# Optimization experiments

Hardware: AMD Instinct MI355X
Metric: run time of the kernel (lower is better)

Reference implementation:

```python
import jax, jax.numpy as jnp
import numpy as np

DIM = 128
CODEBOOK_SCALE = 16384
N_TOKENS = 16384


def setup_inputs() -> dict:
    key = jax.random.key(0)
    k1, k2 = jax.random.split(key)
    x = jax.random.normal(k1, (N_TOKENS, DIM), dtype=jnp.float32)
    codebook = jax.random.normal(k2, (CODEBOOK_SCALE, DIM), dtype=jnp.float32)
    return {"x": x, "codebook": codebook}


def reference(x, codebook):
    # scores: [N, codebook_scale] = x @ codebook.T
    scores = jnp.einsum("nd,cd->nc", x, codebook)
    indices = jnp.argmax(scores, axis=-1)  # [N] int
    loss = jnp.zeros((), dtype=jnp.float32)  # original returns constant 0.0 loss
    return (indices, loss)
```

## Files before the change

### kernel.cpp

```cpp
#include <hip/hip_runtime.h>
#include <hip/hip_bf16.h>

#define NT 16384
#define ND 128
#define NC 16384
#define NSPLIT 8
#define MARGIN 0.4f
#define TILE_BYTES 16384
#define NTILES 32

typedef __bf16 bf16x8 __attribute__((ext_vector_type(8)));
typedef unsigned short u16x8 __attribute__((ext_vector_type(8)));
typedef float f32x4 __attribute__((ext_vector_type(4)));

#define MF __builtin_amdgcn_mfma_f32_16x16x32_bf16

static __device__ __forceinline__ unsigned short f2bf(float f) {
    unsigned u = __float_as_uint(f);
    return (unsigned short)((u + 0x7FFFu + ((u >> 16) & 1u)) >> 16);
}
static __device__ __forceinline__ float bf2f(unsigned short u) {
    return __uint_as_float(((unsigned)u) << 16);
}
static __device__ __forceinline__ bf16x8 u2b(u16x8 u) {
    return __builtin_bit_cast(bf16x8, u);
}
static __device__ __forceinline__ void gl2lds(const void* g, void* l) {
    __builtin_amdgcn_global_load_lds(
        (const __attribute__((address_space(1))) unsigned int*)g,
        (__attribute__((address_space(3))) unsigned int*)l, 16, 0, 0);
}

__global__ __launch_bounds__(256) void lfq_convert_cb(
    const float4* __restrict__ cb4, unsigned short* __restrict__ cbs)
{
    const unsigned i = blockIdx.x * 256 + threadIdx.x;
    const unsigned c = i >> 4;
    const unsigned k = i & 15u;
    const float4 v0 = cb4[i * 2];
    const float4 v1 = cb4[i * 2 + 1];
    const unsigned tile = c >> 6, r = c & 63u;
    const unsigned pos  = (k + r) & 15u;
    u16x8 h;
    h[0] = f2bf(v0.x); h[1] = f2bf(v0.y); h[2] = f2bf(v0.z); h[3] = f2bf(v0.w);
    h[4] = f2bf(v1.x); h[5] = f2bf(v1.y); h[6] = f2bf(v1.z); h[7] = f2bf(v1.w);
    *(u16x8*)(cbs + tile * 8192u + r * 128u + pos * 8u) = h;
}

static __device__ __forceinline__ float exact_dot(
    const float4* __restrict__ xr4, const float* __restrict__ cf, int cidx)
{
    const float4* cr = (const float4*)(cf + (size_t)cidx * ND);
    float a0 = 0.f, a1 = 0.f, a2 = 0.f, a3 = 0.f;
#pragma unroll
    for (int i = 0; i < 32; i += 4) {
        float4 x0 = xr4[i+0], x1 = xr4[i+1], x2 = xr4[i+2], x3 = xr4[i+3];
        float4 c0 = cr[i+0],  c1 = cr[i+1],  c2 = cr[i+2],  c3 = cr[i+3];
        a0 += x0.x*c0.x + x0.y*c0.y + x0.z*c0.z + x0.w*c0.w;
        a1 += x1.x*c1.x + x1.y*c1.y + x1.z*c1.z + x1.w*c1.w;
        a2 += x2.x*c2.x + x2.y*c2.y + x2.z*c2.z + x2.w*c2.w;
        a3 += x3.x*c3.x + x3.y*c3.y + x3.z*c3.z + x3.w*c3.w;
    }
    return (a0 + a1) + (a2 + a3);
}

static __device__ __forceinline__ float exact_dot_g(
    const float* __restrict__ xf, const float* __restrict__ cf,
    int token, int cidx)
{
    const float4* xr = (const float4*)(xf + (size_t)token * ND);
    const float4* cr = (const float4*)(cf + (size_t)cidx * ND);
    float a0 = 0.f, a1 = 0.f, a2 = 0.f, a3 = 0.f;
#pragma unroll
    for (int i = 0; i < 32; i += 4) {
        float4 x0 = xr[i+0], x1 = xr[i+1], x2 = xr[i+2], x3 = xr[i+3];
        float4 c0 = cr[i+0], c1 = cr[i+1], c2 = cr[i+2], c3 = cr[i+3];
        a0 += x0.x*c0.x + x0.y*c0.y + x0.z*c0.z + x0.w*c0.w;
        a1 += x1.x*c1.x + x1.y*c1.y + x1.z*c1.z + x1.w*c1.w;
        a2 += x2.x*c2.x + x2.y*c2.y + x2.z*c2.z + x2.w*c2.w;
        a3 += x3.x*c3.x + x3.y*c3.y + x3.z*c3.z + x3.w*c3.w;
    }
    return (a0 + a1) + (a2 + a3);
}

static __device__ __forceinline__ void top2_upd(
    const f32x4& a, float* b1r, float* b2r, unsigned pk)
{
#pragma unroll
    for (int r4 = 0; r4 < 4; ++r4) {
        float p = __uint_as_float((__float_as_uint(a[r4]) & 0xFFFFFF80u) | pk);
        b2r[r4] = __builtin_amdgcn_fmed3f(p, b1r[r4], b2r[r4]);
        b1r[r4] = fmaxf(p, b1r[r4]);
    }
}

__global__ __launch_bounds__(256)
__attribute__((amdgpu_waves_per_eu(2, 2)))
void lfq_stage1(
    const float* __restrict__ xf, const unsigned short* __restrict__ cbs,
    float* __restrict__ sb1, float* __restrict__ sb2,
    int* __restrict__ si1, int* __restrict__ si2)
{
    const int split = blockIdx.x & 7;
    const int tb    = blockIdx.x >> 3;
    const int t0    = tb * 256;
    const int tid   = threadIdx.x;
    const int w     = tid >> 6;
    const int lane  = tid & 63;
    const int n     = lane & 15;
    const int quad  = lane >> 4;

    __shared__ __attribute__((aligned(16))) unsigned char lds[2 * TILE_BYTES];

    bf16x8 ah[4][4];
#pragma unroll
    for (int tt = 0; tt < 4; ++tt) {
        const float* xr = xf + (size_t)(t0 + w * 64 + tt * 16 + n) * ND + quad * 8;
#pragma unroll
        for (int kk = 0; kk < 4; ++kk) {
            float4 v0 = *(const float4*)(xr + kk * 32);
            float4 v1 = *(const float4*)(xr + kk * 32 + 4);
            u16x8 hu;
            hu[0] = f2bf(v0.x);
            hu[1] = f2bf(v0.y);
            hu[2] = f2bf(v0.z);
            hu[3] = f2bf(v0.w);
            hu[4] = f2bf(v1.x);
            hu[5] = f2bf(v1.y);
            hu[6] = f2bf(v1.z);
            hu[7] = f2bf(v1.w);
            ah[tt][kk] = u2b(hu);
        }
    }

    float b1[4][4], b2[4][4];
#pragma unroll
    for (int tt = 0; tt < 4; ++tt)
#pragma unroll
        for (int r = 0; r < 4; ++r) { b1[tt][r] = -3.0e38f; b2[tt][r] = -3.0e38f; }

    const unsigned char* gtiles =
        (const unsigned char*)cbs + (size_t)(split * NTILES) * TILE_BYTES;
    const unsigned sgo  = (unsigned)(tid * 16);
    const unsigned ldso = (unsigned)(w * 1024);

    const unsigned bb0 = (unsigned)n * 256u + ((((unsigned)(quad + n     )) & 15u) << 4);
    const unsigned bb1 = (unsigned)n * 256u + ((((unsigned)(quad + n +  4)) & 15u) << 4);
    const unsigned bb2 = (unsigned)n * 256u + ((((unsigned)(quad + n +  8)) & 15u) << 4);
    const unsigned bb3 = (unsigned)n * 256u + ((((unsigned)(quad + n + 12)) & 15u) << 4);

    const f32x4 zq = {0.f, 0.f, 0.f, 0.f};

#pragma unroll
    for (int rd = 0; rd < 4; ++rd)
        gl2lds(gtiles + rd * 4096 + sgo, &lds[rd * 4096 + ldso]);
    __syncthreads();

#define PAIR(BUFO, SOFF, PKBASE)                                               \
    {                                                                          \
        bf16x8 qa0 = *(const bf16x8*)&lds[(BUFO) + (SOFF)          + bb0];     \
        bf16x8 qa1 = *(const bf16x8*)&lds[(BUFO) + (SOFF)          + bb1];     \
        bf16x8 qa2 = *(const bf16x8*)&lds[(BUFO) + (SOFF)          + bb2];     \
        bf16x8 qa3 = *(const bf16x8*)&lds[(BUFO) + (SOFF)          + bb3];     \
        bf16x8 qb0 = *(const bf16x8*)&lds[(BUFO) + (SOFF) + 4096u  + bb0];     \
        bf16x8 qb1 = *(const bf16x8*)&lds[(BUFO) + (SOFF) + 4096u  + bb1];     \
        bf16x8 qb2 = *(const bf16x8*)&lds[(BUFO) + (SOFF) + 4096u  + bb2];     \
        bf16x8 qb3 = *(const bf16x8*)&lds[(BUFO) + (SOFF) + 4096u  + bb3];     \
        f32x4 aA0, aA1, aA2, aA3, aB0, aB1, aB2, aB3;                          \
        __builtin_amdgcn_s_setprio(1);                                         \
        aA0 = MF(ah[0][0], qa0, zq,  0,0,0);                                   \
        aA1 = MF(ah[1][0], qa0, zq,  0,0,0);                                   \
        aA2 = MF(ah[2][0], qa0, zq,  0,0,0);                                   \
        aA3 = MF(ah[3][0], qa0, zq,  0,0,0);                                   \
        aB0 = MF(ah[0][0], qb0, zq,  0,0,0);                                   \
        aB1 = MF(ah[1][0], qb0, zq,  0,0,0);                                   \
        aB2 = MF(ah[2][0], qb0, zq,  0,0,0);                                   \
        aB3 = MF(ah[3][0], qb0, zq,  0,0,0);                                   \
        aA0 = MF(ah[0][1], qa1, aA0, 0,0,0);                                   \
        aA1 = MF(ah[1][1], qa1, aA1, 0,0,0);                                   \
        aA2 = MF(ah[2][1], qa1, aA2, 0,0,0);                                   \
        aA3 = MF(ah[3][1], qa1, aA3, 0,0,0);                                   \
        aB0 = MF(ah[0][1], qb1, aB0, 0,0,0);                                   \
        aB1 = MF(ah[1][1], qb1, aB1, 0,0,0);                                   \
        aB2 = MF(ah[2][1], qb1, aB2, 0,0,0);                                   \
        aB3 = MF(ah[3][1], qb1, aB3, 0,0,0);                                   \
        aA0 = MF(ah[0][2], qa2, aA0, 0,0,0);                                   \
        aA1 = MF(ah[1][2], qa2, aA1, 0,0,0);                                   \
        aA2 = MF(ah[2][2], qa2, aA2, 0,0,0);                                   \
        aA3 = MF(ah[3][2], qa2, aA3, 0,0,0);                                   \
        aB0 = MF(ah[0][2], qb2, aB0, 0,0,0);                                   \
        aB1 = MF(ah[1][2], qb2, aB1, 0,0,0);                                   \
        aB2 = MF(ah[2][2], qb2, aB2, 0,0,0);                                   \
        aB3 = MF(ah[3][2], qb2, aB3, 0,0,0);                                   \
        aA0 = MF(ah[0][3], qa3, aA0, 0,0,0);                                   \
        aA1 = MF(ah[1][3], qa3, aA1, 0,0,0);                                   \
        aA2 = MF(ah[2][3], qa3, aA2, 0,0,0);                                   \
        aA3 = MF(ah[3][3], qa3, aA3, 0,0,0);                                   \
        aB0 = MF(ah[0][3], qb3, aB0, 0,0,0);                                   \
        aB1 = MF(ah[1][3], qb3, aB1, 0,0,0);                                   \
        aB2 = MF(ah[2][3], qb3, aB2, 0,0,0);                                   \
        aB3 = MF(ah[3][3], qb3, aB3, 0,0,0);                                   \
        __builtin_amdgcn_s_setprio(0);                                         \
        const unsigned pkA = (unsigned)(127 - (PKBASE));                       \
        const unsigned pkB = (unsigned)(127 - ((PKBASE) + 1));                 \
        top2_upd(aA0, b1[0], b2[0], pkA);                                      \
        top2_upd(aA1, b1[1], b2[1], pkA);                                      \
        top2_upd(aA2, b1[2], b2[2], pkA);                                      \
        top2_upd(aA3, b1[3], b2[3], pkA);                                      \
        top2_upd(aB0, b1[0], b2[0], pkB);                                      \
        top2_upd(aB1, b1[1], b2[1], pkB);                                      \
        top2_upd(aB2, b1[2], b2[2], pkB);                                      \
        top2_upd(aB3, b1[3], b2[3], pkB);                                      \
    }

#define TILE_BODY(T, BUFO, NBO, PREF)                                          \
    {                                                                          \
        if (PREF) {                                                            \
            const unsigned char* g = gtiles + (size_t)((T) + 1) * TILE_BYTES;  \
            gl2lds(g +     0 + sgo, &lds[(NBO)          + ldso]);              \
            gl2lds(g +  4096 + sgo, &lds[(NBO) +  4096u + ldso]);              \
            gl2lds(g +  8192 + sgo, &lds[(NBO) +  8192u + ldso]);              \
            gl2lds(g + 12288 + sgo, &lds[(NBO) + 12288u + ldso]);              \
        }                                                                      \
        PAIR(BUFO, 0u,    (T) * 4)                                             \
        PAIR(BUFO, 8192u, (T) * 4 + 2)                                         \
    }

    for (int t = 0; t < NTILES; t += 2) {
        TILE_BODY(t,     0u,         TILE_BYTES, 1)
        __syncthreads();
        TILE_BODY(t + 1, TILE_BYTES, 0u,         (t + 2 < NTILES))
        __syncthreads();
    }
#undef TILE_BODY
#undef PAIR

    const int cb_base = split * (NC / NSPLIT);
    float v1[4][4], v2[4][4];
    int   c1[4][4], c2[4][4];
#pragma unroll
    for (int tt = 0; tt < 4; ++tt)
#pragma unroll
        for (int r = 0; r < 4; ++r) {
            int j1 = 127 - (int)(__float_as_uint(b1[tt][r]) & 127u);
            int j2 = 127 - (int)(__float_as_uint(b2[tt][r]) & 127u);
            v1[tt][r] = b1[tt][r]; c1[tt][r] = cb_base + j1 * 16 + n;
            v2[tt][r] = b2[tt][r]; c2[tt][r] = cb_base + j2 * 16 + n;
        }

#pragma unroll
    for (int tt = 0; tt < 4; ++tt)
#pragma unroll
        for (int r = 0; r < 4; ++r) {
#pragma unroll
            for (int off = 1; off < 16; off <<= 1) {
                float ob1 = __shfl_xor(v1[tt][r], off, 64);
                int   oi1 = __shfl_xor(c1[tt][r], off, 64);
                float ob2 = __shfl_xor(v2[tt][r], off, 64);
                int   oi2 = __shfl_xor(c2[tt][r], off, 64);
                bool gt = (ob1 > v1[tt][r]) ||
                          (ob1 == v1[tt][r] && oi1 < c1[tt][r]);
                float ls = gt ? v1[tt][r] : ob1;
                int   li = gt ? c1[tt][r] : oi1;
                float ws_ = gt ? ob2 : v2[tt][r];
                int   wi = gt ? oi2 : c2[tt][r];
                bool s2 = (ls > ws_) || (ls == ws_ && li < wi);
                v2[tt][r] = s2 ? ls : ws_;
                c2[tt][r] = s2 ? li : wi;
                v1[tt][r] = gt ? ob1 : v1[tt][r];
                c1[tt][r] = gt ? oi1 : c1[tt][r];
            }
        }

    if (n == 0) {
#pragma unroll
        for (int tt = 0; tt < 4; ++tt)
#pragma unroll
            for (int r = 0; r < 4; ++r) {
                const int token = t0 + w * 64 + tt * 16 + quad * 4 + r;
                const size_t o = (size_t)split * NT + token;
                sb1[o] = v1[tt][r]; si1[o] = c1[tt][r];
                sb2[o] = v2[tt][r]; si2[o] = c2[tt][r];
            }
    }
}

__global__ __launch_bounds__(256) void lfq_combine(
    const float* __restrict__ sb1, const float* __restrict__ sb2,
    const int* __restrict__ si1, const int* __restrict__ si2,
    const float* __restrict__ xf, const float* __restrict__ cf,
    float* __restrict__ out, int out_size)
{
    const int lane = threadIdx.x & 63;
    const int wv   = threadIdx.x >> 6;
    const int g    = lane >> 3;
    const int cl   = lane & 7;
    const int t    = (blockIdx.x * 4 + wv) * 8 + g;

    const size_t o = (size_t)cl * NT + t;
    const float va = sb1[o]; const int ia = si1[o];
    const float vb = sb2[o]; const int ib = si2[o];

    bool lgt = (vb > va) || (vb == va && ib < ia);
    float m  = lgt ? vb : va;
    int   mi = lgt ? ib : ia;
#pragma unroll
    for (int off = 1; off < 8; off <<= 1) {
        float om = __shfl_xor(m, off, 64);
        int   oi = __shfl_xor(mi, off, 64);
        if (om > m || (om == m && oi < mi)) { m = om; mi = oi; }
    }
    const float A1 = m;
    const int   I1 = mi;

    const bool ba = (va >= A1 - MARGIN);
    const bool bb_ = (vb >= A1 - MARGIN);
    int cnt = (ba ? 1 : 0) + (bb_ ? 1 : 0);
#pragma unroll
    for (int off = 1; off < 8; off <<= 1)
        cnt += __shfl_xor(cnt, off, 64);

    int bi = I1;
    if (cnt > 1) {
        float sa = -__builtin_inff(), sb_ = -__builtin_inff();
        if (ba)  sa  = exact_dot_g(xf, cf, t, ia);
        if (bb_) sb_ = exact_dot_g(xf, cf, t, ib);
        bool g2 = (sb_ > sa) || (sb_ == sa && ib < ia);
        float bs = g2 ? sb_ : sa;
        int  bid = g2 ? ib : ia;
#pragma unroll
        for (int off = 1; off < 8; off <<= 1) {
            float os = __shfl_xor(bs, off, 64);
            int   oi = __shfl_xor(bid, off, 64);
            if (os > bs || (os == bs && oi < bid)) { bs = os; bid = oi; }
        }
        bi = bid;
    }
    if (cl == 0) out[t] = (float)bi;
    if (blockIdx.x == 0 && threadIdx.x == 0 && out_size > NT) out[NT] = 0.0f;
}

__global__ __launch_bounds__(512) void lfq_fp32_argmax(
    const float* __restrict__ xf, const float* __restrict__ cf,
    float* __restrict__ out, int out_size)
{
    const int tid = threadIdx.x;
    const int w   = tid >> 6;
    const int tok = tid & 63;
    const int t0  = blockIdx.x * 64;
    __shared__ float s_sc[8][64];
    __shared__ int   s_ix[8][64];

    float4 xr[32];
    const float4* xrow = (const float4*)(xf + (size_t)(t0 + tok) * ND);
#pragma unroll
    for (int i = 0; i < 32; ++i) xr[i] = xrow[i];

    float bs = -__builtin_inff();
    int   bi = 0;
    const int c_begin = w * (NC / 8);
    for (int c = c_begin; c < c_begin + NC / 8; ++c) {
        float s = exact_dot(xr, cf, c);
        if (s > bs) { bs = s; bi = c; }
    }
    s_sc[w][tok] = bs; s_ix[w][tok] = bi;
    __syncthreads();
    if (tid < 64) {
        float bsf = s_sc[0][tid]; int bif = s_ix[0][tid];
#pragma unroll
        for (int ww = 1; ww < 8; ++ww) {
            float s2 = s_sc[ww][tid]; int ii = s_ix[ww][tid];
            if (s2 > bsf || (s2 == bsf && ii < bif)) { bsf = s2; bif = ii; }
        }
        out[t0 + tid] = (float)bif;
    }
    if (blockIdx.x == 0 && tid == 0 && out_size > NT) out[NT] = 0.0f;
}

extern "C" void kernel_launch(void* const* d_in, const int* in_sizes, int n_in,
                              void* d_out, int out_size, void* d_ws, size_t ws_size,
                              hipStream_t stream) {
    const float* x  = (const float*)d_in[0];
    const float* cb = (const float*)d_in[1];
    float* out = (float*)d_out;

    const size_t NCE = (size_t)NC * ND;
    const size_t NEED = NCE * 2 + (size_t)NT * NSPLIT * 4 * 4;
    if (ws_size >= NEED) {
        char* ws = (char*)d_ws;
        unsigned short* cbs = (unsigned short*)ws;
        char* sp = ws + NCE * 2;
        float* sb1 = (float*)sp;
        float* sb2 = (float*)(sp + (size_t)NT * NSPLIT * 4);
        int*   si1 = (int*)  (sp + (size_t)NT * NSPLIT * 8);
        int*   si2 = (int*)  (sp + (size_t)NT * NSPLIT * 12);

        lfq_convert_cb<<<dim3(1024), dim3(256), 0, stream>>>(
            (const float4*)cb, cbs);
        lfq_stage1<<<dim3((NT / 256) * NSPLIT), dim3(256), 0, stream>>>(
            x, cbs, sb1, sb2, si1, si2);
        lfq_combine<<<dim3(NT / 32), dim3(256), 0, stream>>>(
            sb1, sb2, si1, si2, x, cb, out, out_size);
    } else {
        lfq_fp32_argmax<<<dim3(NT / 64), dim3(512), 0, stream>>>(x, cb, out, out_size);
    }
}
```

Baseline: 161.9 us.

## Load codebook fragments directly from global into registers, dropping LDS staging

The codebook preprocessing now writes bf16 data in an MFMA-fragment-ordered layout, so each lane can fetch its B operands with coalesced 16-byte global loads. The stage-1 loop drops the LDS double buffer, global_load_lds and __syncthreads, and instead software-pipelines register loads of the next codebook pair while computing the current one. This removes block-wide barriers and LDS traffic. In exchange, each of the four waves in a block now loads the same codebook data separately, relying on L1/L2 to absorb the redundancy, and register pressure rises.

Result: faster. 156.8 us (-3.1%).

```diff
diff --git a/kernel.cpp b/kernel.cpp
--- a/kernel.cpp
+++ b/kernel.cpp
@@ -6,8 +6,6 @@
 #define NC 16384
 #define NSPLIT 8
 #define MARGIN 0.4f
-#define TILE_BYTES 16384
-#define NTILES 32
 
 typedef __bf16 bf16x8 __attribute__((ext_vector_type(8)));
 typedef unsigned short u16x8 __attribute__((ext_vector_type(8)));
@@ -25,26 +23,28 @@
 static __device__ __forceinline__ bf16x8 u2b(u16x8 u) {
     return __builtin_bit_cast(bf16x8, u);
 }
-static __device__ __forceinline__ void gl2lds(const void* g, void* l) {
-    __builtin_amdgcn_global_load_lds(
-        (const __attribute__((address_space(1))) unsigned int*)g,
-        (__attribute__((address_space(3))) unsigned int*)l, 16, 0, 0);
-}
 
 __global__ __launch_bounds__(256) void lfq_convert_cb(
     const float4* __restrict__ cb4, unsigned short* __restrict__ cbs)
 {
     const unsigned i = blockIdx.x * 256 + threadIdx.x;
-    const unsigned c = i >> 4;
-    const unsigned k = i & 15u;
+    const unsigned c  = i >> 4;
+    const unsigned k8 = i & 15u;
     const float4 v0 = cb4[i * 2];
     const float4 v1 = cb4[i * 2 + 1];
-    const unsigned tile = c >> 6, r = c & 63u;
-    const unsigned pos  = (k + r) & 15u;
+    const unsigned split = c >> 11;
+    const unsigned cl    = c & 2047u;
+    const unsigned pair  = cl >> 5;
+    const unsigned sp    = (cl >> 4) & 1u;
+    const unsigned n     = cl & 15u;
+    const unsigned k     = k8 >> 2;
+    const unsigned quad  = k8 & 3u;
+    const unsigned idx = split * 262144u + pair * 4096u + sp * 2048u +
+                         k * 512u + quad * 128u + n * 8u;
     u16x8 h;
     h[0] = f2bf(v0.x); h[1] = f2bf(v0.y); h[2] = f2bf(v0.z); h[3] = f2bf(v0.w);
     h[4] = f2bf(v1.x); h[5] = f2bf(v1.y); h[6] = f2bf(v1.z); h[7] = f2bf(v1.w);
-    *(u16x8*)(cbs + tile * 8192u + r * 128u + pos * 8u) = h;
+    *(u16x8*)(cbs + idx) = h;
 }
 
 static __device__ __forceinline__ float exact_dot(
@@ -109,8 +109,6 @@
     const int lane  = tid & 63;
     const int n     = lane & 15;
     const int quad  = lane >> 4;
-
-    __shared__ __attribute__((aligned(16))) unsigned char lds[2 * TILE_BYTES];
 
     bf16x8 ah[4][4];
 #pragma unroll
@@ -139,70 +137,61 @@
 #pragma unroll
         for (int r = 0; r < 4; ++r) { b1[tt][r] = -3.0e38f; b2[tt][r] = -3.0e38f; }
 
-    const unsigned char* gtiles =
-        (const unsigned char*)cbs + (size_t)(split * NTILES) * TILE_BYTES;
-    const unsigned sgo  = (unsigned)(tid * 16);
-    const unsigned ldso = (unsigned)(w * 1024);
-
-    const unsigned bb0 = (unsigned)n * 256u + ((((unsigned)(quad + n     )) & 15u) << 4);
-    const unsigned bb1 = (unsigned)n * 256u + ((((unsigned)(quad + n +  4)) & 15u) << 4);
-    const unsigned bb2 = (unsigned)n * 256u + ((((unsigned)(quad + n +  8)) & 15u) << 4);
-    const unsigned bb3 = (unsigned)n * 256u + ((((unsigned)(quad + n + 12)) & 15u) << 4);
+    const unsigned char* gp =
+        (const unsigned char*)cbs + (size_t)split * 524288u +
+        (unsigned)lane * 16u;
 
     const f32x4 zq = {0.f, 0.f, 0.f, 0.f};
 
-#pragma unroll
-    for (int rd = 0; rd < 4; ++rd)
-        gl2lds(gtiles + rd * 4096 + sgo, &lds[rd * 4096 + ldso]);
-    __syncthreads();
-
-#define PAIR(BUFO, SOFF, PKBASE)                                               \
+#define LOADPAIR(Q0,Q1,Q2,Q3,Q4,Q5,Q6,Q7, G)                                   \
+    Q0 = *(const bf16x8*)((G));                                                \
+    Q1 = *(const bf16x8*)((G) + 1024);                                         \
+    Q2 = *(const bf16x8*)((G) + 2048);                                         \
+    Q3 = *(const bf16x8*)((G) + 3072);                                         \
+    Q4 = *(const bf16x8*)((G) + 4096);                                         \
+    Q5 = *(const bf16x8*)((G) + 5120);                                         \
+    Q6 = *(const bf16x8*)((G) + 6144);                                         \
+    Q7 = *(const bf16x8*)((G) + 7168);
+
+#define COMPUTE(Q0,Q1,Q2,Q3,Q4,Q5,Q6,Q7, P)                                    \
     {                                                                          \
-        bf16x8 qa0 = *(const bf16x8*)&lds[(BUFO) + (SOFF)          + bb0];     \
-        bf16x8 qa1 = *(const bf16x8*)&lds[(BUFO) + (SOFF)          + bb1];     \
-        bf16x8 qa2 = *(const bf16x8*)&lds[(BUFO) + (SOFF)          + bb2];     \
-        bf16x8 qa3 = *(const bf16x8*)&lds[(BUFO) + (SOFF)          + bb3];     \
-        bf16x8 qb0 = *(const bf16x8*)&lds[(BUFO) + (SOFF) + 4096u  + bb0];     \
-        bf16x8 qb1 = *(const bf16x8*)&lds[(BUFO) + (SOFF) + 4096u  + bb1];     \
-        bf16x8 qb2 = *(const bf16x8*)&lds[(BUFO) + (SOFF) + 4096u  + bb2];     \
-        bf16x8 qb3 = *(const bf16x8*)&lds[(BUFO) + (SOFF) + 4096u  + bb3];     \
         f32x4 aA0, aA1, aA2, aA3, aB0, aB1, aB2, aB3;                          \
         __builtin_amdgcn_s_setprio(1);                                         \
-        aA0 = MF(ah[0][0], qa0, zq,  0,0,0);                                   \
-        aA1 = MF(ah[1][0], qa0, zq,  0,0,0);                                   \
-        aA2 = MF(ah[2][0], qa0, zq,  0,0,0);                                   \
-        aA3 = MF(ah[3][0], qa0, zq,  0,0,0);                                   \
-        aB0 = MF(ah[0][0], qb0, zq,  0,0,0);                                   \
-        aB1 = MF(ah[1][0], qb0, zq,  0,0,0);                                   \
-        aB2 = MF(ah[2][0], qb0, zq,  0,0,0);                                   \
-        aB3 = MF(ah[3][0], qb0, zq,  0,0,0);                                   \
-        aA0 = MF(ah[0][1], qa1, aA0, 0,0,0);                                   \
-        aA1 = MF(ah[1][1], qa1, aA1, 0,0,0);                                   \
-        aA2 = MF(ah[2][1], qa1, aA2, 0,0,0);                                   \
-        aA3 = MF(ah[3][1], qa1, aA3, 0,0,0);                                   \
-        aB0 = MF(ah[0][1], qb1, aB0, 0,0,0);                                   \
-        aB1 = MF(ah[1][1], qb1, aB1, 0,0,0);                                   \
-        aB2 = MF(ah[2][1], qb1, aB2, 0,0,0);                                   \
-        aB3 = MF(ah[3][1], qb1, aB3, 0,0,0);                                   \
-        aA0 = MF(ah[0][2], qa2, aA0, 0,0,0);                                   \
-        aA1 = MF(ah[1][2], qa2, aA1, 0,0,0);                                   \
-        aA2 = MF(ah[2][2], qa2, aA2, 0,0,0);                                   \
-        aA3 = MF(ah[3][2], qa2, aA3, 0,0,0);                                   \
-        aB0 = MF(ah[0][2], qb2, aB0, 0,0,0);                                   \
-        aB1 = MF(ah[1][2], qb2, aB1, 0,0,0);                                   \
-        aB2 = MF(ah[2][2], qb2, aB2, 0,0,0);                                   \
-        aB3 = MF(ah[3][2], qb2, aB3, 0,0,0);                                   \
-        aA0 = MF(ah[0][3], qa3, aA0, 0,0,0);                                   \
-        aA1 = MF(ah[1][3], qa3, aA1, 0,0,0);                                   \
-        aA2 = MF(ah[2][3], qa3, aA2, 0,0,0);                                   \
-        aA3 = MF(ah[3][3], qa3, aA3, 0,0,0);                                   \
-        aB0 = MF(ah[0][3], qb3, aB0, 0,0,0);                                   \
-        aB1 = MF(ah[1][3], qb3, aB1, 0,0,0);                                   \
-        aB2 = MF(ah[2][3], qb3, aB2, 0,0,0);                                   \
-        aB3 = MF(ah[3][3], qb3, aB3, 0,0,0);                                   \
+        aA0 = MF(ah[0][0], Q0, zq,  0,0,0);                                    \
+        aA1 = MF(ah[1][0], Q0, zq,  0,0,0);                                    \
+        aA2 = MF(ah[2][0], Q0, zq,  0,0,0);                                    \
+        aA3 = MF(ah[3][0], Q0, zq,  0,0,0);                                    \
+        aB0 = MF(ah[0][0], Q4, zq,  0,0,0);                                    \
+        aB1 = MF(ah[1][0], Q4, zq,  0,0,0);                                    \
+        aB2 = MF(ah[2][0], Q4, zq,  0,0,0);                                    \
+        aB3 = MF(ah[3][0], Q4, zq,  0,0,0);                                    \
+        aA0 = MF(ah[0][1], Q1, aA0, 0,0,0);                                    \
+        aA1 = MF(ah[1][1], Q1, aA1, 0,0,0);                                    \
+        aA2 = MF(ah[2][1], Q1, aA2, 0,0,0);                                    \
+        aA3 = MF(ah[3][1], Q1, aA3, 0,0,0);                                    \
+        aB0 = MF(ah[0][1], Q5, aB0, 0,0,0);                                    \
+        aB1 = MF(ah[1][1], Q5, aB1, 0,0,0);                                    \
+        aB2 = MF(ah[2][1], Q5, aB2, 0,0,0);                                    \
+        aB3 = MF(ah[3][1], Q5, aB3, 0,0,0);                                    \
+        aA0 = MF(ah[0][2], Q2, aA0, 0,0,0);                                    \
+        aA1 = MF(ah[1][2], Q2, aA1, 0,0,0);                                    \
+        aA2 = MF(ah[2][2], Q2, aA2, 0,0,0);                                    \
+        aA3 = MF(ah[3][2], Q2, aA3, 0,0,0);                                    \
+        aB0 = MF(ah[0][2], Q6, aB0, 0,0,0);                                    \
+        aB1 = MF(ah[1][2], Q6, aB1, 0,0,0);                                    \
+        aB2 = MF(ah[2][2], Q6, aB2, 0,0,0);                                    \
+        aB3 = MF(ah[3][2], Q6, aB3, 0,0,0);                                    \
+        aA0 = MF(ah[0][3], Q3, aA0, 0,0,0);                                    \
+        aA1 = MF(ah[1][3], Q3, aA1, 0,0,0);                                    \
+        aA2 = MF(ah[2][3], Q3, aA2, 0,0,0);                                    \
+        aA3 = MF(ah[3][3], Q3, aA3, 0,0,0);                                    \
+        aB0 = MF(ah[0][3], Q7, aB0, 0,0,0);                                    \
+        aB1 = MF(ah[1][3], Q7, aB1, 0,0,0);                                    \
+        aB2 = MF(ah[2][3], Q7, aB2, 0,0,0);                                    \
+        aB3 = MF(ah[3][3], Q7, aB3, 0,0,0);                                    \
         __builtin_amdgcn_s_setprio(0);                                         \
-        const unsigned pkA = (unsigned)(127 - (PKBASE));                       \
-        const unsigned pkB = (unsigned)(127 - ((PKBASE) + 1));                 \
+        const unsigned pkA = (unsigned)(127 - (P) * 2);                        \
+        const unsigned pkB = (unsigned)(127 - (P) * 2 - 1);                    \
         top2_upd(aA0, b1[0], b2[0], pkA);                                      \
         top2_upd(aA1, b1[1], b2[1], pkA);                                      \
         top2_upd(aA2, b1[2], b2[2], pkA);                                      \
@@ -213,27 +202,23 @@
         top2_upd(aB3, b1[3], b2[3], pkB);                                      \
     }
 
-#define TILE_BODY(T, BUFO, NBO, PREF)                                          \
-    {                                                                          \
-        if (PREF) {                                                            \
-            const unsigned char* g = gtiles + (size_t)((T) + 1) * TILE_BYTES;  \
-            gl2lds(g +     0 + sgo, &lds[(NBO)          + ldso]);              \
-            gl2lds(g +  4096 + sgo, &lds[(NBO) +  4096u + ldso]);              \
-            gl2lds(g +  8192 + sgo, &lds[(NBO) +  8192u + ldso]);              \
-            gl2lds(g + 12288 + sgo, &lds[(NBO) + 12288u + ldso]);              \
-        }                                                                      \
-        PAIR(BUFO, 0u,    (T) * 4)                                             \
-        PAIR(BUFO, 8192u, (T) * 4 + 2)                                         \
-    }
-
-    for (int t = 0; t < NTILES; t += 2) {
-        TILE_BODY(t,     0u,         TILE_BYTES, 1)
-        __syncthreads();
-        TILE_BODY(t + 1, TILE_BYTES, 0u,         (t + 2 < NTILES))
-        __syncthreads();
-    }
-#undef TILE_BODY
-#undef PAIR
+    bf16x8 qa0, qa1, qa2, qa3, qa4, qa5, qa6, qa7;
+    bf16x8 qb0, qb1, qb2, qb3, qb4, qb5, qb6, qb7;
+
+    LOADPAIR(qa0,qa1,qa2,qa3,qa4,qa5,qa6,qa7, gp)
+
+    for (int p = 0; p < 62; p += 2) {
+        LOADPAIR(qb0,qb1,qb2,qb3,qb4,qb5,qb6,qb7, gp + (p + 1) * 8192)
+        COMPUTE (qa0,qa1,qa2,qa3,qa4,qa5,qa6,qa7, p)
+        LOADPAIR(qa0,qa1,qa2,qa3,qa4,qa5,qa6,qa7, gp + (p + 2) * 8192)
+        COMPUTE (qb0,qb1,qb2,qb3,qb4,qb5,qb6,qb7, p + 1)
+    }
+    LOADPAIR(qb0,qb1,qb2,qb3,qb4,qb5,qb6,qb7, gp + 63 * 8192)
+    COMPUTE (qa0,qa1,qa2,qa3,qa4,qa5,qa6,qa7, 62)
+    COMPUTE (qb0,qb1,qb2,qb3,qb4,qb5,qb6,qb7, 63)
+
+#undef LOADPAIR
+#undef COMPUTE
 
     const int cb_base = split * (NC / NSPLIT);
     float v1[4][4], v2[4][4];
```
